# Kernel optimization log

Measured on AMD Instinct MI355X. Metric: run time of the kernel, lower is better.

## Reference

```python
import jax, jax.numpy as jnp
import numpy as np

N_BINS = 64
EPS = 0.001
T_MIN = 0.0
T_MAX = 1.0


def setup_inputs() -> dict:
    key = jax.random.key(0)
    k_t, k_lt, k_lu = jax.random.split(key, 3)
    t = jax.random.uniform(k_t, (32, 4096), dtype=jnp.float32)
    # learned per-bin logits, initialized like torch (zeros - log(n_bins)) plus noise
    base = -jnp.float32(np.log(N_BINS))
    l_t = base + 0.1 * jax.random.normal(k_lt, (N_BINS,), dtype=jnp.float32)
    l_u = base + 0.1 * jax.random.normal(k_lu, (N_BINS,), dtype=jnp.float32)
    return {"t": t, "l_t": l_t, "l_u": l_u}


def reference(t, l_t, l_u):
    # Per-bin weights (params are shared across all (n,l) positions, so compute once
    # on the 1-D bin axis and broadcast -- same math as expanding first).
    w_t = jax.nn.softmax(l_t) + EPS
    w_t = w_t / jnp.sum(w_t)
    w_u = jnp.exp(l_u) + EPS
    w_u = w_u / jnp.sum(w_u)  # normalized=True

    zero = jnp.zeros((1,), dtype=w_t.dtype)
    e_t = jnp.concatenate([zero, jnp.cumsum(w_t)])  # [n_bins+1]
    e_u = jnp.concatenate([zero, jnp.cumsum(w_u)])  # [n_bins+1]

    t_prime = (t - T_MIN) / (T_MAX - T_MIN)  # [n, l]
    # bucket search: count knots <= t', then clamp
    idx = jnp.sum((e_t[None, None, :] <= t_prime[:, :, None]).astype(jnp.int32), axis=-1) - 1
    idx = jnp.clip(idx, 0, N_BINS - 1)  # [n, l]

    et0 = e_t[idx]
    et1 = e_t[idx + 1]
    eu0 = e_u[idx]
    eu1 = e_u[idx + 1]
    u = eu0 + (eu1 - eu0) * ((t_prime - et0) / (et1 - et0))
    return u
```

## Files before the change

### kernel.cpp

```cpp
#include <hip/hip_runtime.h>
#include <math.h>

#define N_BINS 64
#define EPS_W 0.001f

__device__ inline float wave_sum(float v) {
    #pragma unroll
    for (int off = 32; off >= 1; off >>= 1) v += __shfl_xor(v, off, 64);
    return v;
}
__device__ inline float wave_max(float v) {
    #pragma unroll
    for (int off = 32; off >= 1; off >>= 1) v = fmaxf(v, __shfl_xor(v, off, 64));
    return v;
}
__device__ inline float wave_scan_incl(float v, int lane) {
    #pragma unroll
    for (int off = 1; off < 64; off <<= 1) {
        float o = __shfl_up(v, off, 64);
        if (lane >= off) v += o;
    }
    return v;
}

__device__ inline float interp_one(float tp, const float* __restrict__ s_et,
                                   const float* __restrict__ s_eu) {
    int idx = 0;
    #pragma unroll
    for (int s = 32; s; s >>= 1) {
        int cand = idx + s;
        idx = (s_et[cand] <= tp) ? cand : idx;
    }
    float et0 = s_et[idx];
    float et1 = s_et[idx + 1];
    float eu0 = s_eu[idx];
    float eu1 = s_eu[idx + 1];
    return eu0 + (eu1 - eu0) * ((tp - et0) / (et1 - et0));
}

__global__ __launch_bounds__(256) void losscdf_kernel(
    const float* __restrict__ t,
    const float* __restrict__ l_t,
    const float* __restrict__ l_u,
    float* __restrict__ out,
    int n)
{
    __shared__ float s_et[N_BINS + 1];
    __shared__ float s_eu[N_BINS + 1];

    if (threadIdx.x < 64) {
        int lane = threadIdx.x;
        float lt = l_t[lane];
        float lu = l_u[lane];

        float m  = wave_max(lt);
        float ex = expf(lt - m);
        float se = wave_sum(ex);
        float wt = ex / se + EPS_W;
        float swt = wave_sum(wt);
        wt = wt / swt;

        float eu = expf(lu) + EPS_W;
        float seu = wave_sum(eu);
        float wu = eu / seu;

        float ct = wave_scan_incl(wt, lane);
        float cu = wave_scan_incl(wu, lane);

        if (lane == 0) { s_et[0] = 0.0f; s_eu[0] = 0.0f; }
        s_et[lane + 1] = ct;
        s_eu[lane + 1] = cu;
    }
    __syncthreads();

    int n4 = n >> 2;
    const float4* __restrict__ t4 = (const float4*)t;
    float4* __restrict__ o4 = (float4*)out;
    int stride = gridDim.x * blockDim.x;
    for (int i = blockIdx.x * blockDim.x + threadIdx.x; i < n4; i += stride) {
        float4 v = t4[i];
        float4 r;
        r.x = interp_one(v.x, s_et, s_eu);
        r.y = interp_one(v.y, s_et, s_eu);
        r.z = interp_one(v.z, s_et, s_eu);
        r.w = interp_one(v.w, s_et, s_eu);
        o4[i] = r;
    }

    int tail = n & 3;
    if (tail && blockIdx.x == 0 && (int)threadIdx.x < tail) {
        int i = (n4 << 2) + threadIdx.x;
        out[i] = interp_one(t[i], s_et, s_eu);
    }
}

extern "C" void kernel_launch(void* const* d_in, const int* in_sizes, int n_in,
                              void* d_out, int out_size, void* d_ws, size_t ws_size,
                              hipStream_t stream) {
    const float* t   = (const float*)d_in[0];
    const float* l_t = (const float*)d_in[1];
    const float* l_u = (const float*)d_in[2];
    float* out = (float*)d_out;
    int n = in_sizes[0];
    int n4 = n >> 2;
    int block = 256;
    int grid = (n4 + block - 1) / block;
    if (grid < 1) grid = 1;
    losscdf_kernel<<<grid, block, 0, stream>>>(t, l_t, l_u, out, n);
}
```

Before: 57.99 us.

## Replace per-element binary search with LUT-guided lookup and precomputed bin slopes

Builds a 256-entry lookup table of starting bin indices plus per-bin packed (et0, eu0, slope) records in shared memory, so each element does a table lookup, a short linear walk, and one FMA instead of a 6-step binary search and a divide. It also drops float4 vectorization to one element per thread, which launches four times as many blocks. Each of those blocks repeats the softmax/scan prologue and adds an extra LUT build and barrier, raising fixed per-block overhead. Precomputing the slope changes the rounding slightly compared with the reference divide.

```diff
diff --git a/kernel.cpp b/kernel.cpp
--- a/kernel.cpp
+++ b/kernel.cpp
@@ -3,6 +3,7 @@
 
 #define N_BINS 64
 #define EPS_W 0.001f
+#define LUT_SIZE 256
 
 __device__ inline float wave_sum(float v) {
     #pragma unroll
@@ -23,21 +24,6 @@
     return v;
 }
 
-__device__ inline float interp_one(float tp, const float* __restrict__ s_et,
-                                   const float* __restrict__ s_eu) {
-    int idx = 0;
-    #pragma unroll
-    for (int s = 32; s; s >>= 1) {
-        int cand = idx + s;
-        idx = (s_et[cand] <= tp) ? cand : idx;
-    }
-    float et0 = s_et[idx];
-    float et1 = s_et[idx + 1];
-    float eu0 = s_eu[idx];
-    float eu1 = s_eu[idx + 1];
-    return eu0 + (eu1 - eu0) * ((tp - et0) / (et1 - et0));
-}
-
 __global__ __launch_bounds__(256) void losscdf_kernel(
     const float* __restrict__ t,
     const float* __restrict__ l_t,
@@ -45,8 +31,9 @@
     float* __restrict__ out,
     int n)
 {
-    __shared__ float s_et[N_BINS + 1];
-    __shared__ float s_eu[N_BINS + 1];
+    __shared__ float  s_et[N_BINS + 1];
+    __shared__ float4 s_bin[N_BINS];
+    __shared__ int    s_lut[LUT_SIZE];
 
     if (threadIdx.x < 64) {
         int lane = threadIdx.x;
@@ -67,30 +54,44 @@
         float ct = wave_scan_incl(wt, lane);
         float cu = wave_scan_incl(wu, lane);
 
-        if (lane == 0) { s_et[0] = 0.0f; s_eu[0] = 0.0f; }
+        if (lane == 0) s_et[0] = 0.0f;
         s_et[lane + 1] = ct;
-        s_eu[lane + 1] = cu;
+
+        float et0 = ct - wt;
+        float et1 = ct;
+        float eu0 = cu - wu;
+        float eu1 = cu;
+        if (lane == 0) { et0 = 0.0f; eu0 = 0.0f; }
+        float4 b;
+        b.x = et0;
+        b.y = eu0;
+        b.z = (eu1 - eu0) / (et1 - et0);
+        b.w = et1;
+        s_bin[lane] = b;
     }
     __syncthreads();
 
-    int n4 = n >> 2;
-    const float4* __restrict__ t4 = (const float4*)t;
-    float4* __restrict__ o4 = (float4*)out;
-    int stride = gridDim.x * blockDim.x;
-    for (int i = blockIdx.x * blockDim.x + threadIdx.x; i < n4; i += stride) {
-        float4 v = t4[i];
-        float4 r;
-        r.x = interp_one(v.x, s_et, s_eu);
-        r.y = interp_one(v.y, s_et, s_eu);
-        r.z = interp_one(v.z, s_et, s_eu);
-        r.w = interp_one(v.w, s_et, s_eu);
-        o4[i] = r;
+    {
+        float slot_lo = (float)threadIdx.x * (1.0f / LUT_SIZE);
+        int idx = 0;
+        #pragma unroll
+        for (int s = 32; s; s >>= 1) {
+            int cand = idx + s;
+            idx = (s_et[cand] <= slot_lo) ? cand : idx;
+        }
+        s_lut[threadIdx.x] = idx;
     }
+    __syncthreads();
 
-    int tail = n & 3;
-    if (tail && blockIdx.x == 0 && (int)threadIdx.x < tail) {
-        int i = (n4 << 2) + threadIdx.x;
-        out[i] = interp_one(t[i], s_et, s_eu);
+    int i = blockIdx.x * blockDim.x + threadIdx.x;
+    if (i < n) {
+        float tp = t[i];
+        int k = (int)(tp * (float)LUT_SIZE);
+        k = min(max(k, 0), LUT_SIZE - 1);
+        int idx = s_lut[k];
+        while (idx < N_BINS - 1 && s_et[idx + 1] <= tp) idx++;
+        float4 b = s_bin[idx];
+        out[i] = fmaf(b.z, tp - b.x, b.y);
     }
 }
 
@@ -102,9 +103,8 @@
     const float* l_u = (const float*)d_in[2];
     float* out = (float*)d_out;
     int n = in_sizes[0];
-    int n4 = n >> 2;
     int block = 256;
-    int grid = (n4 + block - 1) / block;
+    int grid = (n + block - 1) / block;
     if (grid < 1) grid = 1;
     losscdf_kernel<<<grid, block, 0, stream>>>(t, l_t, l_u, out, n);
 }
```

Measured after the change: 57.92 us. No clear change (-0.1%).
